# Performance work log

Hardware: AMD Instinct MI355X
Metric: run time of the kernel (lower is better)

Reference implementation:

```python
import jax, jax.numpy as jnp
import numpy as np

# Topology constants (fixed DAG ontology)
B = 16384          # batch
IN_DIM = 4096      # input_dim
N_LEAF = 64        # leaf terms with direct input maps
IPL = 64           # inputs per leaf (disjoint slices; one-hot connection mask -> diag weights)
N_MID = 16         # mid-level modules
CPM = 4            # leaf children per mid module
MID_N = 128        # neurons per mid module
OUT = 256          # output_dim at root


def setup_inputs() -> dict:
    key = jax.random.key(0)
    k = jax.random.split(key, 7)
    return {
        "x": jax.random.normal(k[0], (B, IN_DIM), jnp.float32),
        # input-layer kernels: only the masked diagonal entries of each [IN_DIM, IPL]
        # kernel are nonzero after kernel*connections, so store them as [N_LEAF, IPL]
        "w_inp": jax.random.normal(k[1], (N_LEAF, IPL), jnp.float32) * 0.1,
        "pbias": jnp.ones((N_LEAF,), jnp.float32),  # pbias=1.0 per input layer
        "W_mid": jax.random.normal(k[2], (N_MID, CPM * IPL, MID_N), jnp.float32) * 0.05,
        "b_mid": jnp.zeros((N_MID, MID_N), jnp.float32),
        "W_root": jax.random.normal(k[3], (N_MID * MID_N, OUT), jnp.float32) * 0.05,
        "b_root": jnp.zeros((OUT,), jnp.float32),
    }


def reference(x, w_inp, pbias, W_mid, b_mid, W_root, b_root):
    b = x.shape[0]
    # Leaf input layers: gather each leaf's input slice, multiply by its diagonal
    # kernel entries (== dot(x, kernel*one_hot_mask)), linear act, add pbias.
    leaf = x.reshape(b, N_LEAF, IPL) * w_inp + pbias[:, None]          # [B, N_LEAF, IPL]
    # Mid modules: concat CPM leaf children -> masked-dense (mask all ones) + bias + tanh
    mid_in = leaf.reshape(b, N_MID, CPM * IPL)                          # [B, N_MID, 256]
    mid = jnp.tanh(jnp.einsum('bgi,gio->bgo', mid_in, W_mid) + b_mid)   # [B, N_MID, 128]
    # Root module: concat all mid children -> dense + bias, linear output activation
    out = mid.reshape(b, N_MID * MID_N) @ W_root + b_root               # [B, OUT]
    return out
```

## Files before the change

kernel.cpp:

```cpp
#include <hip/hip_runtime.h>

typedef __attribute__((ext_vector_type(8))) short short8;
typedef __attribute__((ext_vector_type(4))) float floatx4;
typedef unsigned short ushort_t;
typedef unsigned int uint32;


__device__ __forceinline__ uint32 f2bf_bits(float f) {
  uint32 u = __builtin_bit_cast(uint32, f);
  u += 0x7fffu + ((u >> 16) & 1u);
  return u >> 16;
}

__device__ __forceinline__ float tanh_fast(float x) {
  float e = __expf(2.0f * x);
  return 1.0f - 2.0f * __builtin_amdgcn_rcpf(e + 1.0f);
}

__device__ __forceinline__ void gl_lds16(const void* g, void* l) {
  __builtin_amdgcn_global_load_lds((const __attribute__((address_space(1))) void*)g,
                                   (__attribute__((address_space(3))) void*)l,
                                   16, 0, 0);
}


__global__ __launch_bounds__(256) void prep(const float* __restrict__ w_inp,
                                            const float* __restrict__ pbias,
                                            const float* __restrict__ W_mid,
                                            const float* __restrict__ b_mid,
                                            const float* __restrict__ W_root,
                                            ushort_t* __restrict__ Wtm,
                                            ushort_t* __restrict__ Wtr,
                                            float* __restrict__ bias_eff) {
  const int b = blockIdx.x, t = threadIdx.x;
  if (b < 2048) {
    const int idx = b * 256 + t;
    const int g = idx >> 15;
    const int rem = idx & 32767;
    const int i = rem >> 7;
    const int o = rem & 127;
    const float v = W_mid[(g << 15) + i * 128 + o] * w_inp[g * 256 + i];
    Wtm[(g << 15) + o * 256 + i] = (ushort_t)f2bf_bits(v);
  } else if (b < 4096) {
    const int idx = (b - 2048) * 256 + t;
    const int k = idx >> 8;
    const int o = idx & 255;
    Wtr[o * 2048 + k] = (ushort_t)f2bf_bits(W_root[k * 256 + o]);
  } else {
    const int idx = (b - 4096) * 256 + t;
    const int g = idx >> 7;
    const int o = idx & 127;
    float s = b_mid[idx];
    for (int i = 0; i < 256; ++i)
      s += pbias[g * 4 + (i >> 6)] * W_mid[(g << 15) + i * 128 + o];
    bias_eff[idx] = s;
  }
}


__global__ __launch_bounds__(256) void midk(const float* __restrict__ x,
                                            const ushort_t* __restrict__ Wtm,
                                            const float* __restrict__ bias_eff,
                                            ushort_t* __restrict__ mid) {
  __shared__ __align__(16) unsigned char smem[34816];
  ushort_t* sA = (ushort_t*)smem;
  ushort_t* sB = (ushort_t*)(smem + 10240);

  const int t = threadIdx.x;
  const int lane = t & 63;
  const int wv = __builtin_amdgcn_readfirstlane(t >> 6);
  const int g = blockIdx.y;
  const int m0 = blockIdx.x * 128;

  const int wm = (wv & 1) * 64;
  const int wn = (wv >> 1) * 64;

  const int ar = t >> 1, ah = t & 1;
  const float* agp = x + (m0 + ar) * 4096 + g * 256 + ah * 16;
  ushort_t* asw = sA + ar * 40 + ah * 16;

  const ushort_t* bgp = Wtm + (g << 15) + (wv * 32 + (lane >> 2)) * 256 + (lane & 3) * 8;
  ushort_t* bl = sB + (wv * 32) * 32;

  floatx4 acc[4][4] = {};

  for (int kk = 0; kk < 8; ++kk) {
    __syncthreads();
    gl_lds16(bgp + kk * 32, bl);
    gl_lds16(bgp + 16 * 256 + kk * 32, bl + 16 * 32);

    const float4* ap4 = (const float4*)(agp + kk * 32);
    float4 f0 = ap4[0], f1 = ap4[1], f2 = ap4[2], f3 = ap4[3];
    uint32 u0 = f2bf_bits(f0.x) | (f2bf_bits(f0.y) << 16);
    uint32 u1 = f2bf_bits(f0.z) | (f2bf_bits(f0.w) << 16);
    uint32 u2 = f2bf_bits(f1.x) | (f2bf_bits(f1.y) << 16);
    uint32 u3 = f2bf_bits(f1.z) | (f2bf_bits(f1.w) << 16);
    uint32 u4 = f2bf_bits(f2.x) | (f2bf_bits(f2.y) << 16);
    uint32 u5 = f2bf_bits(f2.z) | (f2bf_bits(f2.w) << 16);
    uint32 u6 = f2bf_bits(f3.x) | (f2bf_bits(f3.y) << 16);
    uint32 u7 = f2bf_bits(f3.z) | (f2bf_bits(f3.w) << 16);
    ((uint4*)asw)[0] = make_uint4(u0, u1, u2, u3);
    ((uint4*)asw)[1] = make_uint4(u4, u5, u6, u7);
    __syncthreads();

    short8 af[4], bfrag[4];
#pragma unroll
    for (int mi = 0; mi < 4; ++mi)
      af[mi] = *(const short8*)(sA + (wm + mi * 16 + (lane & 15)) * 40 + (lane >> 4) * 8);
#pragma unroll
    for (int ni = 0; ni < 4; ++ni)
      bfrag[ni] = *(const short8*)(sB + (wn + ni * 16 + (lane & 15)) * 32 + (lane >> 4) * 8);
#pragma unroll
    for (int mi = 0; mi < 4; ++mi)
#pragma unroll
      for (int ni = 0; ni < 4; ++ni)
        acc[mi][ni] = __builtin_amdgcn_mfma_f32_16x16x32_bf16(af[mi], bfrag[ni], acc[mi][ni], 0, 0, 0);
  }

  __syncthreads();
  ushort_t* sC = (ushort_t*)smem;
#pragma unroll
  for (int ni = 0; ni < 4; ++ni) {
    const int col = wn + ni * 16 + (lane & 15);
    const float bias = bias_eff[g * 128 + col];
#pragma unroll
    for (int mi = 0; mi < 4; ++mi) {
#pragma unroll
      for (int r = 0; r < 4; ++r) {
        const int row = wm + mi * 16 + (lane >> 4) * 4 + r;
        sC[row * 136 + col] = (ushort_t)f2bf_bits(tanh_fast(acc[mi][ni][r] + bias));
      }
    }
  }
  __syncthreads();
  const int rr = t >> 1, hh = t & 1;
  const uint4* src = (const uint4*)(sC + rr * 136 + hh * 64);
  uint4* dst = (uint4*)(mid + (m0 + rr) * 2048 + g * 128 + hh * 64);
#pragma unroll
  for (int i = 0; i < 8; ++i) dst[i] = src[i];
}


__global__ __launch_bounds__(256) void rootk(const ushort_t* __restrict__ mid,
                                             const ushort_t* __restrict__ Wtr,
                                             const float* __restrict__ b_root,
                                             float* __restrict__ out) {
  __shared__ __align__(16) ushort_t sA[128 * 32];
  __shared__ __align__(16) ushort_t sB[128 * 32];

  const int t = threadIdx.x;
  const int lane = t & 63;
  const int wv = __builtin_amdgcn_readfirstlane(t >> 6);
  const int m0 = blockIdx.x * 128;
  const int n0 = blockIdx.y * 128;
  const int kz = blockIdx.z;

  const int wm = (wv & 1) * 64;
  const int wn = (wv >> 1) * 64;

  const ushort_t* ag = mid + (m0 + wv * 32 + (lane >> 2)) * 2048 + kz * 1024 + (lane & 3) * 8;
  const ushort_t* bg = Wtr + (n0 + wv * 32 + (lane >> 2)) * 2048 + kz * 1024 + (lane & 3) * 8;
  ushort_t* al = sA + (wv * 32) * 32;
  ushort_t* bl = sB + (wv * 32) * 32;

  floatx4 acc[4][4] = {};

  for (int kk = 0; kk < 32; ++kk) {
    __syncthreads();
    gl_lds16(ag + kk * 32, al);
    gl_lds16(ag + 16 * 2048 + kk * 32, al + 16 * 32);
    gl_lds16(bg + kk * 32, bl);
    gl_lds16(bg + 16 * 2048 + kk * 32, bl + 16 * 32);
    __syncthreads();

    short8 af[4], bfrag[4];
#pragma unroll
    for (int mi = 0; mi < 4; ++mi)
      af[mi] = *(const short8*)(sA + (wm + mi * 16 + (lane & 15)) * 32 + (lane >> 4) * 8);
#pragma unroll
    for (int ni = 0; ni < 4; ++ni)
      bfrag[ni] = *(const short8*)(sB + (wn + ni * 16 + (lane & 15)) * 32 + (lane >> 4) * 8);
#pragma unroll
    for (int mi = 0; mi < 4; ++mi)
#pragma unroll
      for (int ni = 0; ni < 4; ++ni)
        acc[mi][ni] = __builtin_amdgcn_mfma_f32_16x16x32_bf16(af[mi], bfrag[ni], acc[mi][ni], 0, 0, 0);
  }

#pragma unroll
  for (int ni = 0; ni < 4; ++ni) {
    const int col = n0 + wn + ni * 16 + (lane & 15);
    const float br = (kz == 0) ? b_root[col] : 0.0f;
#pragma unroll
    for (int mi = 0; mi < 4; ++mi)
#pragma unroll
      for (int r = 0; r < 4; ++r) {
        const int row = m0 + wm + mi * 16 + (lane >> 4) * 4 + r;
        atomicAdd(out + row * 256 + col, acc[mi][ni][r] + br);
      }
  }
}


extern "C" void kernel_launch(void* const* d_in, const int* in_sizes, int n_in,
                              void* d_out, int out_size, void* d_ws, size_t ws_size,
                              hipStream_t stream) {
  const float* x      = (const float*)d_in[0];
  const float* w_inp  = (const float*)d_in[1];
  const float* pbias  = (const float*)d_in[2];
  const float* W_mid  = (const float*)d_in[3];
  const float* b_mid  = (const float*)d_in[4];
  const float* W_root = (const float*)d_in[5];
  const float* b_root = (const float*)d_in[6];
  float* out = (float*)d_out;

  char* ws = (char*)d_ws;
  ushort_t* Wtm      = (ushort_t*)(ws);
  ushort_t* Wtr      = (ushort_t*)(ws + (1 << 20));
  float*    bias_eff = (float*)   (ws + (2 << 20));
  ushort_t* midbuf   = (ushort_t*)(ws + (4 << 20));

  hipMemsetAsync(d_out, 0, (size_t)out_size * sizeof(float), stream);
  prep<<<dim3(4104), dim3(256), 0, stream>>>(w_inp, pbias, W_mid, b_mid, W_root, Wtm, Wtr, bias_eff);
  midk<<<dim3(128, 16), dim3(256), 0, stream>>>(x, Wtm, bias_eff, midbuf);
  rootk<<<dim3(128, 2, 2), dim3(256), 0, stream>>>(midbuf, Wtr, b_root, out);
}
```

Measured before the change: 475.4 us.

## Replace root split-K atomics with partial buffers and a separate reduce kernel

```diff
diff --git a/kernel.cpp b/kernel.cpp
--- a/kernel.cpp
+++ b/kernel.cpp
@@ -47,13 +47,18 @@
     const int o = idx & 255;
     Wtr[o * 2048 + k] = (ushort_t)f2bf_bits(W_root[k * 256 + o]);
   } else {
-    const int idx = (b - 4096) * 256 + t;
-    const int g = idx >> 7;
-    const int o = idx & 127;
-    float s = b_mid[idx];
-    for (int i = 0; i < 256; ++i)
-      s += pbias[g * 4 + (i >> 6)] * W_mid[(g << 15) + i * 128 + o];
-    bias_eff[idx] = s;
+    const int g = b - 4096;
+    const int o = t;
+    if (o < 128) {
+      float s = b_mid[g * 128 + o];
+      const float* wp = W_mid + (g << 15) + o;
+      float pb[4];
+#pragma unroll
+      for (int q = 0; q < 4; ++q) pb[q] = pbias[g * 4 + q];
+#pragma unroll 8
+      for (int i = 0; i < 256; ++i) s += pb[i >> 6] * wp[i * 128];
+      bias_eff[g * 128 + o] = s;
+    }
   }
 }
 
@@ -143,8 +148,7 @@
 
 __global__ __launch_bounds__(256) void rootk(const ushort_t* __restrict__ mid,
                                              const ushort_t* __restrict__ Wtr,
-                                             const float* __restrict__ b_root,
-                                             float* __restrict__ out) {
+                                             float* __restrict__ partial) {
   __shared__ __align__(16) ushort_t sA[128 * 32];
   __shared__ __align__(16) ushort_t sB[128 * 32];
 
@@ -187,18 +191,31 @@
         acc[mi][ni] = __builtin_amdgcn_mfma_f32_16x16x32_bf16(af[mi], bfrag[ni], acc[mi][ni], 0, 0, 0);
   }
 
+  float* pout = partial + (size_t)kz * (16384 * 256);
 #pragma unroll
   for (int ni = 0; ni < 4; ++ni) {
     const int col = n0 + wn + ni * 16 + (lane & 15);
-    const float br = (kz == 0) ? b_root[col] : 0.0f;
 #pragma unroll
     for (int mi = 0; mi < 4; ++mi)
 #pragma unroll
       for (int r = 0; r < 4; ++r) {
         const int row = m0 + wm + mi * 16 + (lane >> 4) * 4 + r;
-        atomicAdd(out + row * 256 + col, acc[mi][ni][r] + br);
+        pout[row * 256 + col] = acc[mi][ni][r];
       }
   }
+}
+
+
+__global__ __launch_bounds__(256) void reducek(const float* __restrict__ partial,
+                                               const float* __restrict__ b_root,
+                                               float* __restrict__ out) {
+  const int i4 = (blockIdx.x * 256 + threadIdx.x) * 4;
+  float4 a = *(const float4*)(partial + i4);
+  float4 b = *(const float4*)(partial + (16384 * 256) + i4);
+  float4 c = *(const float4*)(b_root + (i4 & 255));
+  float4 r = make_float4(a.x + b.x + c.x, a.y + b.y + c.y,
+                         a.z + b.z + c.z, a.w + b.w + c.w);
+  *(float4*)(out + i4) = r;
 }
 
 
@@ -219,9 +236,10 @@
   ushort_t* Wtr      = (ushort_t*)(ws + (1 << 20));
   float*    bias_eff = (float*)   (ws + (2 << 20));
   ushort_t* midbuf   = (ushort_t*)(ws + (4 << 20));
-
-  hipMemsetAsync(d_out, 0, (size_t)out_size * sizeof(float), stream);
-  prep<<<dim3(4104), dim3(256), 0, stream>>>(w_inp, pbias, W_mid, b_mid, W_root, Wtm, Wtr, bias_eff);
+  float*    partials = (float*)   (ws + (72u << 20));
+
+  prep<<<dim3(4112), dim3(256), 0, stream>>>(w_inp, pbias, W_mid, b_mid, W_root, Wtm, Wtr, bias_eff);
   midk<<<dim3(128, 16), dim3(256), 0, stream>>>(x, Wtm, bias_eff, midbuf);
-  rootk<<<dim3(128, 2, 2), dim3(256), 0, stream>>>(midbuf, Wtr, b_root, out);
-}
+  rootk<<<dim3(128, 2, 2), dim3(256), 0, stream>>>(midbuf, Wtr, partials);
+  reducek<<<dim3(4096), dim3(256), 0, stream>>>(partials, b_root, out);
+}
```

Measured after the change: 463.2 us. 1.03x faster.
